# Kernel optimization log

Hardware: AMD Instinct MI355X
Metric: run time of the kernel (lower is better)

Reference implementation:

```python
import jax, jax.numpy as jnp
import numpy as np

LMAX = 5
DIMS = [2 * l + 1 for l in range(LMAX + 1)]
S = sum(d * d for d in DIMS)  # 286 = sum_l (2l+1)^2 (mul_l = dim_l = 2l+1)
F_IN, F_OUT = 128, 128
B = 512
N_GRID = 512


def setup_inputs() -> dict:
    key = jax.random.key(0)
    k1, k2, k3 = jax.random.split(key, 3)
    # x: signal over SO(3) irreps, shape (B, f_in, S)
    x = jax.random.normal(k1, (B, F_IN, S), dtype=jnp.float32)
    # w: learned spatial filter, shape (f_in, f_out, n_grid) (nn.Parameter, normal init)
    w = jax.random.normal(k2, (F_IN, F_OUT, N_GRID), dtype=jnp.float32)
    # D: flattened Wigner-D buffer, shape (n_grid, S). Stand-in random values;
    # the forward math is identical to the true Wigner-D buffer.
    D = jax.random.normal(k3, (N_GRID, S), dtype=jnp.float32)
    return {"x": x, "w": w, "D": D}


def _so3_linear(x, psi):
    """e3nn o3.Linear over so3_irreps(LMAX) with external weights psi.

    Per degree l: x_l (B, f_in, 2l+1 [mul], 2l+1 [dim]),
    psi_l (f_in, f_out, mul_in, mul_out); mix multiplicities and f channels,
    with fan-in normalization 1/sqrt(f_in * mul_in).
    """
    bsz = x.shape[0]
    outs = []
    off = 0
    for l in range(LMAX + 1):
        d = 2 * l + 1
        blk = d * d
        x_l = x[:, :, off:off + blk].reshape(bsz, F_IN, d, d)
        w_l = psi[:, :, off:off + blk].reshape(F_IN, F_OUT, d, d)
        scale = 1.0 / np.sqrt(F_IN * d).astype(np.float32)
        y_l = jnp.einsum('bxui,xyuv->byvi', x_l, w_l) * scale
        outs.append(y_l.reshape(bsz, F_OUT, blk))
        off += blk
    return jnp.concatenate(outs, axis=-1)


def reference(x, w, D):
    # project spatial filter into harmonic (Fourier) domain
    psi = jnp.einsum('ni,xyn->xyi', D, w) / np.float32(np.sqrt(N_GRID))
    return _so3_linear(x, psi)
```

## Files before the change

kernel.cpp:

```cpp
#include <hip/hip_runtime.h>
#include <hip/hip_bf16.h>


#define NT 256
#define NTILES 1144
#define NWORKERS 768
typedef __bf16 bf16x8 __attribute__((ext_vector_type(8)));
typedef float f32x4 __attribute__((ext_vector_type(4)));
typedef unsigned int u32;

__device__ __forceinline__ void gload_lds16(const void* g, void* l) {
  __builtin_amdgcn_global_load_lds(
      (const __attribute__((address_space(1))) u32*)g,
      (__attribute__((address_space(3))) u32*)l, 16, 0, 0);
}

__device__ __forceinline__ void decode_s(int s, int& off, int& d) {
  if (s >= 165)      { off = 165; d = 11; }
  else if (s >= 84)  { off = 84;  d = 9; }
  else if (s >= 35)  { off = 35;  d = 7; }
  else if (s >= 10)  { off = 10;  d = 5; }
  else if (s >= 1)   { off = 1;   d = 3; }
  else               { off = 0;   d = 1; }
}

__device__ __forceinline__ void stage_tile(
    const __hip_bfloat16* __restrict__ Ap, const __hip_bfloat16* __restrict__ Bp,
    int LDK, int ktv, int m0, int n0, int tid, int wave,
    __hip_bfloat16* sA, __hip_bfloat16* sB) {
#pragma unroll
  for (int c = 0; c < 4; ++c) {
    const int q = c * 256 + tid;
    const int row = q >> 3, slot = q & 7;
    const int scol = ((slot ^ (row & 7)) << 3);
    gload_lds16(&Ap[(m0 + row) * LDK + ktv + scol], &sA[(c * 256 + wave * 64) << 3]);
    gload_lds16(&Bp[(n0 + row) * LDK + ktv + scol], &sB[(c * 256 + wave * 64) << 3]);
  }
}

__device__ __forceinline__ void load_frags(
    const __hip_bfloat16* sA, const __hip_bfloat16* sB,
    int wr, int wc, int r15, int khi, bf16x8 (&af)[4][2], bf16x8 (&bf)[4][2]) {
#pragma unroll
  for (int m = 0; m < 4; ++m)
#pragma unroll
    for (int kk = 0; kk < 2; ++kk) {
      const int row = wr * 64 + m * 16 + r15;
      const int slot = (kk * 4 + khi) ^ (row & 7);
      af[m][kk] = *reinterpret_cast<const bf16x8*>(&sA[row * 64 + slot * 8]);
    }
#pragma unroll
  for (int n = 0; n < 4; ++n)
#pragma unroll
    for (int kk = 0; kk < 2; ++kk) {
      const int row = wc * 64 + n * 16 + r15;
      const int slot = (kk * 4 + khi) ^ (row & 7);
      bf[n][kk] = *reinterpret_cast<const bf16x8*>(&sB[row * 64 + slot * 8]);
    }
}

__device__ __forceinline__ void do_mfma(
    const bf16x8 (&af)[4][2], const bf16x8 (&bf)[4][2], f32x4 (&acc)[4][4]) {
#pragma unroll
  for (int kk = 0; kk < 2; ++kk)
#pragma unroll
    for (int m = 0; m < 4; ++m)
#pragma unroll
      for (int n = 0; n < 4; ++n)
        acc[m][n] = __builtin_amdgcn_mfma_f32_16x16x32_bf16(
            af[m][kk], bf[n][kk], acc[m][n], 0, 0, 0);
}

__global__ __launch_bounds__(NT)
void prep(const float* __restrict__ w, const float* __restrict__ Dm,
          __hip_bfloat16* __restrict__ wb, __hip_bfloat16* __restrict__ DT,
          int* __restrict__ cnt) {
  const int bx = blockIdx.x;
  if (bx == 0 && threadIdx.x == 0) *cnt = 0;
  if (bx < 4096) {
    const int t = bx * NT + threadIdx.x;
    const float4 a = reinterpret_cast<const float4*>(w)[t * 2];
    const float4 b = reinterpret_cast<const float4*>(w)[t * 2 + 1];
    __hip_bfloat16 v[8];
    v[0] = __float2bfloat16(a.x); v[1] = __float2bfloat16(a.y);
    v[2] = __float2bfloat16(a.z); v[3] = __float2bfloat16(a.w);
    v[4] = __float2bfloat16(b.x); v[5] = __float2bfloat16(b.y);
    v[6] = __float2bfloat16(b.z); v[7] = __float2bfloat16(b.w);
    *reinterpret_cast<bf16x8*>(&wb[t * 8]) = *reinterpret_cast<bf16x8*>(v);
  } else {
    const int e = (bx - 4096) * NT + threadIdx.x;
    const int s = e >> 9, g = e & 511;
    DT[e] = (s < 286) ? __float2bfloat16(Dm[g * 286 + s]) : __float2bfloat16(0.0f);
  }
}

__global__ __launch_bounds__(NT)
void psi_mfma(const __hip_bfloat16* __restrict__ wb,
              const __hip_bfloat16* __restrict__ DT,
              __hip_bfloat16* __restrict__ PT) {
  const int m0 = blockIdx.x * 128, n0 = blockIdx.y * 128;

  __shared__ __hip_bfloat16 sA[2][128 * 64];
  __shared__ __hip_bfloat16 sB[2][128 * 64];

  const int tid = threadIdx.x;
  const int lane = tid & 63, wave = tid >> 6;
  const int wr = wave & 1, wc = wave >> 1;
  const int r15 = lane & 15, khi = lane >> 4;

  f32x4 acc[4][4] = {};
  bf16x8 af[4][2], bf[4][2];

  stage_tile(wb, DT, 512, 0, m0, n0, tid, wave, sA[0], sB[0]);
  __syncthreads();
  int cur = 0;
  for (int t = 0; t < 8; ++t) {
    if (t + 1 < 8)
      stage_tile(wb, DT, 512, (t + 1) << 6, m0, n0, tid, wave, sA[cur ^ 1], sB[cur ^ 1]);
    load_frags(sA[cur], sB[cur], wr, wc, r15, khi, af, bf);
    do_mfma(af, bf, acc);
    if (t + 1 < 8) { __syncthreads(); cur ^= 1; }
  }

#pragma unroll
  for (int n = 0; n < 4; ++n) {
    const int s = n0 + wc * 64 + n * 16 + r15;
    if (s >= 286) continue;
    int off, d;
    decode_s(s, off, d);
    const int rel = s - off;
    const int u = rel / d, v = rel - u * d;
    const float scale = 1.0f / (256.0f * sqrtf((float)d));
    __hip_bfloat16* Pl = PT + off * 16384;
    const int Kd = 128 * d;
#pragma unroll
    for (int m = 0; m < 4; ++m)
#pragma unroll
      for (int j = 0; j < 4; ++j) {
        const int row = m0 + wr * 64 + m * 16 + khi * 4 + j;
        const int x = row >> 7, y = row & 127;
        Pl[(y * d + v) * Kd + (x * d + u)] = __float2bfloat16(acc[m][n][j] * scale);
      }
  }
}

template<int D, int OFF>
__device__ __forceinline__ void build_one(const float* __restrict__ X,
                                          __hip_bfloat16* __restrict__ A,
                                          int b, __hip_bfloat16* sm) {
  const float* src = X + (size_t)b * (128 * 286) + OFF;
  for (int e = threadIdx.x; e < 128 * D * D; e += NT) {
    const int x = e / (D * D), r = e - x * (D * D);
    sm[e] = __float2bfloat16(src[x * 286 + r]);
  }
  __syncthreads();
  __hip_bfloat16* dst = A + (size_t)65536 * OFF + (size_t)b * (D * 128 * D);
  for (int o = threadIdx.x; o < D * 128 * D; o += NT) {
    const int i = o / (128 * D);
    const int rem = o - i * (128 * D);
    const int x = rem / D, u = rem - x * D;
    dst[o] = sm[x * D * D + u * D + i];
  }
}

__global__ __launch_bounds__(NT)
void build_A_all(const float* __restrict__ X, __hip_bfloat16* __restrict__ A) {
  __shared__ __hip_bfloat16 sm[128 * 121];
  const int bx = blockIdx.x;
  if (bx < 512)       build_one<11, 165>(X, A, bx, sm);
  else if (bx < 1024) build_one<9, 84>(X, A, bx - 512, sm);
  else if (bx < 1536) build_one<7, 35>(X, A, bx - 1024, sm);
  else if (bx < 2048) build_one<5, 10>(X, A, bx - 1536, sm);
  else if (bx < 2560) build_one<3, 1>(X, A, bx - 2048, sm);
  else                build_one<1, 0>(X, A, bx - 2560, sm);
}

__global__ __launch_bounds__(NT)
void main_gemm(const __hip_bfloat16* __restrict__ Aall,
               const __hip_bfloat16* __restrict__ PTall,
               float* __restrict__ out, int* __restrict__ cnt) {
  __shared__ __hip_bfloat16 sA[128 * 64];
  __shared__ __hip_bfloat16 sB[128 * 64];
  __shared__ int s_tile;

  const int tid = threadIdx.x;
  const int lane = tid & 63, wave = tid >> 6;
  const int wr = wave & 1, wc = wave >> 1;
  const int r15 = lane & 15, khi = lane >> 4;

  for (;;) {
    if (tid == 0) s_tile = atomicAdd(cnt, 1);
    __syncthreads();
    int bx = s_tile;
    if (bx >= NTILES) return;

    int off, d;
    if (bx < 484)       { off = 165; d = 11; }
    else if (bx < 808)  { off = 84;  d = 9;  bx -= 484; }
    else if (bx < 1004) { off = 35;  d = 7;  bx -= 808; }
    else if (bx < 1104) { off = 10;  d = 5;  bx -= 1004; }
    else if (bx < 1140) { off = 1;   d = 3;  bx -= 1104; }
    else                { off = 0;   d = 1;  bx -= 1140; }
    const int bm = bx % (4 * d);
    const int bn = bx / (4 * d);
    const int Kn = 128 * d;
    const __hip_bfloat16* A  = Aall  + 65536 * off;
    const __hip_bfloat16* BT = PTall + 16384 * off;
    const int m0 = bm * 128, n0 = bn * 128;

    f32x4 acc[4][4] = {};
    bf16x8 af[4][2], bf[4][2];

    const int nk = Kn >> 6;
    for (int t = 0; t < nk; ++t) {
      stage_tile(A, BT, Kn, t << 6, m0, n0, tid, wave, sA, sB);
      __syncthreads();
      load_frags(sA, sB, wr, wc, r15, khi, af, bf);
      do_mfma(af, bf, acc);
      if (t + 1 < nk) __syncthreads();
    }

    int yo4[4], v4[4];
#pragma unroll
    for (int n = 0; n < 4; ++n) {
      const int col = n0 + wc * 64 + n * 16 + r15;
      yo4[n] = col / d;
      v4[n] = col - yo4[n] * d;
    }
#pragma unroll
    for (int m = 0; m < 4; ++m)
#pragma unroll
      for (int j = 0; j < 4; ++j) {
        const int row = m0 + wr * 64 + m * 16 + khi * 4 + j;
        const int bb = row / d, i = row - bb * d;
        float* orow = out + (size_t)bb * 36608 + off + i;
#pragma unroll
        for (int n = 0; n < 4; ++n)
          orow[yo4[n] * 286 + v4[n] * d] = acc[m][n][j];
      }
  }
}

extern "C" void kernel_launch(void* const* d_in, const int* in_sizes, int n_in,
                              void* d_out, int out_size, void* d_ws, size_t ws_size,
                              hipStream_t stream) {
  const float* x  = (const float*)d_in[0];
  const float* w  = (const float*)d_in[1];
  const float* Dm = (const float*)d_in[2];
  float* out = (float*)d_out;

  __hip_bfloat16* PT = (__hip_bfloat16*)d_ws;
  __hip_bfloat16* A  = PT + 16384 * 286;
  __hip_bfloat16* wb = A + 65536 * 286;
  __hip_bfloat16* DT = wb + 16384 * 512;
  int* cnt = (int*)(DT + 384 * 512);

  prep<<<dim3(4864), dim3(NT), 0, stream>>>(w, Dm, wb, DT, cnt);
  psi_mfma<<<dim3(128, 3), dim3(NT), 0, stream>>>(wb, DT, PT);
  build_A_all<<<dim3(3072), dim3(NT), 0, stream>>>(x, A);
  main_gemm<<<dim3(NWORKERS), dim3(NT), 0, stream>>>(A, PT, out, cnt);
}
```

Baseline: 167.3 us.

## Enlarge main GEMM tiles to 256x256 with 512-thread blocks and edge masking

The main GEMM moves from 128x128 tiles with 4 waves to 256x256 tiles with 8 waves, each wave computing a 128x64 sub-tile. Staging and fragment loads are inlined with an XOR swizzle. B rows past N are clamped and output columns past N are masked, because 128*d is not a multiple of 256. The aim is to raise data reuse and cut global/LDS traffic per FLOP. The cost is higher register use, padded wasted work, and fewer tiles (322) to spread across CUs.

Result: no change. 170.1 us (+1.7%).

```diff
diff --git a/kernel.cpp b/kernel.cpp
--- a/kernel.cpp
+++ b/kernel.cpp
@@ -3,8 +3,9 @@
 
 
 #define NT 256
-#define NTILES 1144
-#define NWORKERS 768
+#define NT2 512
+#define NTILES2 322
+#define NWORKERS 512
 typedef __bf16 bf16x8 __attribute__((ext_vector_type(8)));
 typedef float f32x4 __attribute__((ext_vector_type(4)));
 typedef unsigned int u32;
@@ -175,68 +176,105 @@
   else                build_one<1, 0>(X, A, bx - 2560, sm);
 }
 
-__global__ __launch_bounds__(NT)
+__global__ __launch_bounds__(NT2)
 void main_gemm(const __hip_bfloat16* __restrict__ Aall,
                const __hip_bfloat16* __restrict__ PTall,
                float* __restrict__ out, int* __restrict__ cnt) {
-  __shared__ __hip_bfloat16 sA[128 * 64];
-  __shared__ __hip_bfloat16 sB[128 * 64];
+  __shared__ __hip_bfloat16 sA[256 * 64];
+  __shared__ __hip_bfloat16 sB[256 * 64];
   __shared__ int s_tile;
 
   const int tid = threadIdx.x;
   const int lane = tid & 63, wave = tid >> 6;
-  const int wr = wave & 1, wc = wave >> 1;
+  const int wr = wave >> 2, wc = wave & 3;
   const int r15 = lane & 15, khi = lane >> 4;
 
   for (;;) {
     if (tid == 0) s_tile = atomicAdd(cnt, 1);
     __syncthreads();
     int bx = s_tile;
-    if (bx >= NTILES) return;
-
-    int off, d;
-    if (bx < 484)       { off = 165; d = 11; }
-    else if (bx < 808)  { off = 84;  d = 9;  bx -= 484; }
-    else if (bx < 1004) { off = 35;  d = 7;  bx -= 808; }
-    else if (bx < 1104) { off = 10;  d = 5;  bx -= 1004; }
-    else if (bx < 1140) { off = 1;   d = 3;  bx -= 1104; }
-    else                { off = 0;   d = 1;  bx -= 1140; }
-    const int bm = bx % (4 * d);
-    const int bn = bx / (4 * d);
-    const int Kn = 128 * d;
+    if (bx >= NTILES2) return;
+
+    int off, d, nbn;
+    if (bx < 132)      { off = 165; d = 11; nbn = 6; }
+    else if (bx < 222) { off = 84;  d = 9;  nbn = 5; bx -= 132; }
+    else if (bx < 278) { off = 35;  d = 7;  nbn = 4; bx -= 222; }
+    else if (bx < 308) { off = 10;  d = 5;  nbn = 3; bx -= 278; }
+    else if (bx < 320) { off = 1;   d = 3;  nbn = 2; bx -= 308; }
+    else               { off = 0;   d = 1;  nbn = 1; bx -= 320; }
+    const int bn = bx % nbn;
+    const int bm = bx / nbn;
+    const int Kn = 128 * d, Nn = 128 * d;
     const __hip_bfloat16* A  = Aall  + 65536 * off;
     const __hip_bfloat16* BT = PTall + 16384 * off;
-    const int m0 = bm * 128, n0 = bn * 128;
-
-    f32x4 acc[4][4] = {};
-    bf16x8 af[4][2], bf[4][2];
+    const int m0 = bm * 256, n0 = bn * 256;
+
+    f32x4 acc[8][4] = {};
 
     const int nk = Kn >> 6;
     for (int t = 0; t < nk; ++t) {
-      stage_tile(A, BT, Kn, t << 6, m0, n0, tid, wave, sA, sB);
+      const int kt = t << 6;
+#pragma unroll
+      for (int c = 0; c < 4; ++c) {
+        const int q = c * 512 + tid;
+        const int row = q >> 3, slot = q & 7;
+        const int scol = ((slot ^ (row & 7)) << 3);
+        gload_lds16(&A[(m0 + row) * Kn + kt + scol],
+                    &sA[(c * 512 + wave * 64) << 3]);
+        int brow = n0 + row;
+        if (brow >= Nn) brow = Nn - 1;
+        gload_lds16(&BT[brow * Kn + kt + scol],
+                    &sB[(c * 512 + wave * 64) << 3]);
+      }
       __syncthreads();
-      load_frags(sA, sB, wr, wc, r15, khi, af, bf);
-      do_mfma(af, bf, acc);
+
+      bf16x8 bfr[4][2];
+#pragma unroll
+      for (int n = 0; n < 4; ++n)
+#pragma unroll
+        for (int kk = 0; kk < 2; ++kk) {
+          const int row = wc * 64 + n * 16 + r15;
+          const int slot = (kk * 4 + khi) ^ (row & 7);
+          bfr[n][kk] = *reinterpret_cast<const bf16x8*>(&sB[row * 64 + slot * 8]);
+        }
+#pragma unroll
+      for (int m = 0; m < 8; ++m) {
+        bf16x8 afr[2];
+#pragma unroll
+        for (int kk = 0; kk < 2; ++kk) {
+          const int row = wr * 128 + m * 16 + r15;
+          const int slot = (kk * 4 + khi) ^ (row & 7);
+          afr[kk] = *reinterpret_cast<const bf16x8*>(&sA[row * 64 + slot * 8]);
+        }
+#pragma unroll
+        for (int kk = 0; kk < 2; ++kk)
+#pragma unroll
+          for (int n = 0; n < 4; ++n)
+            acc[m][n] = __builtin_amdgcn_mfma_f32_16x16x32_bf16(
+                afr[kk], bfr[n][kk], acc[m][n], 0, 0, 0);
+      }
       if (t + 1 < nk) __syncthreads();
     }
 
-    int yo4[4], v4[4];
+    int yo4[4], v4[4], cok[4];
 #pragma unroll
     for (int n = 0; n < 4; ++n) {
       const int col = n0 + wc * 64 + n * 16 + r15;
-      yo4[n] = col / d;
-      v4[n] = col - yo4[n] * d;
+      cok[n] = (col < Nn);
+      const int cc = cok[n] ? col : 0;
+      yo4[n] = cc / d;
+      v4[n] = cc - yo4[n] * d;
     }
 #pragma unroll
-    for (int m = 0; m < 4; ++m)
+    for (int m = 0; m < 8; ++m)
 #pragma unroll
       for (int j = 0; j < 4; ++j) {
-        const int row = m0 + wr * 64 + m * 16 + khi * 4 + j;
+        const int row = m0 + wr * 128 + m * 16 + khi * 4 + j;
         const int bb = row / d, i = row - bb * d;
         float* orow = out + (size_t)bb * 36608 + off + i;
 #pragma unroll
         for (int n = 0; n < 4; ++n)
-          orow[yo4[n] * 286 + v4[n] * d] = acc[m][n][j];
+          if (cok[n]) orow[yo4[n] * 286 + v4[n] * d] = acc[m][n][j];
       }
   }
 }
@@ -258,5 +296,5 @@
   prep<<<dim3(4864), dim3(NT), 0, stream>>>(w, Dm, wb, DT, cnt);
   psi_mfma<<<dim3(128, 3), dim3(NT), 0, stream>>>(wb, DT, PT);
   build_A_all<<<dim3(3072), dim3(NT), 0, stream>>>(x, A);
-  main_gemm<<<dim3(NWORKERS), dim3(NT), 0, stream>>>(A, PT, out, cnt);
-}
+  main_gemm<<<dim3(NWORKERS), dim3(NT2), 0, stream>>>(A, PT, out, cnt);
+}
```

## Stage GEMM epilogue through LDS for coalesced writes, fuse A-build into prep

Applied to the files above, without the earlier changes.

The main GEMM epilogue now writes accumulators to a padded LDS buffer and scatters them to global memory in output-index order, so stores to the strided output layout coalesce better than direct per-lane scattered stores. The tile body is templated on degree so K and loop counts become compile-time constants. The separate build_A kernel is merged into the prep kernel, removing one launch. LDS use rises to about 33KB and extra synchronisation plus a bounds-checked loop are added in the epilogue.

After: 179.4 us. 7.2% more time.

```diff
diff --git a/kernel.cpp b/kernel.cpp
--- a/kernel.cpp
+++ b/kernel.cpp
@@ -24,57 +24,31 @@
   else               { off = 0;   d = 1; }
 }
 
-__device__ __forceinline__ void stage_tile(
-    const __hip_bfloat16* __restrict__ Ap, const __hip_bfloat16* __restrict__ Bp,
-    int LDK, int ktv, int m0, int n0, int tid, int wave,
-    __hip_bfloat16* sA, __hip_bfloat16* sB) {
-#pragma unroll
-  for (int c = 0; c < 4; ++c) {
-    const int q = c * 256 + tid;
-    const int row = q >> 3, slot = q & 7;
-    const int scol = ((slot ^ (row & 7)) << 3);
-    gload_lds16(&Ap[(m0 + row) * LDK + ktv + scol], &sA[(c * 256 + wave * 64) << 3]);
-    gload_lds16(&Bp[(n0 + row) * LDK + ktv + scol], &sB[(c * 256 + wave * 64) << 3]);
-  }
-}
-
-__device__ __forceinline__ void load_frags(
-    const __hip_bfloat16* sA, const __hip_bfloat16* sB,
-    int wr, int wc, int r15, int khi, bf16x8 (&af)[4][2], bf16x8 (&bf)[4][2]) {
-#pragma unroll
-  for (int m = 0; m < 4; ++m)
-#pragma unroll
-    for (int kk = 0; kk < 2; ++kk) {
-      const int row = wr * 64 + m * 16 + r15;
-      const int slot = (kk * 4 + khi) ^ (row & 7);
-      af[m][kk] = *reinterpret_cast<const bf16x8*>(&sA[row * 64 + slot * 8]);
-    }
-#pragma unroll
-  for (int n = 0; n < 4; ++n)
-#pragma unroll
-    for (int kk = 0; kk < 2; ++kk) {
-      const int row = wc * 64 + n * 16 + r15;
-      const int slot = (kk * 4 + khi) ^ (row & 7);
-      bf[n][kk] = *reinterpret_cast<const bf16x8*>(&sB[row * 64 + slot * 8]);
-    }
-}
-
-__device__ __forceinline__ void do_mfma(
-    const bf16x8 (&af)[4][2], const bf16x8 (&bf)[4][2], f32x4 (&acc)[4][4]) {
-#pragma unroll
-  for (int kk = 0; kk < 2; ++kk)
-#pragma unroll
-    for (int m = 0; m < 4; ++m)
-#pragma unroll
-      for (int n = 0; n < 4; ++n)
-        acc[m][n] = __builtin_amdgcn_mfma_f32_16x16x32_bf16(
-            af[m][kk], bf[n][kk], acc[m][n], 0, 0, 0);
+template<int D, int OFF>
+__device__ __forceinline__ void build_one(const float* __restrict__ X,
+                                          __hip_bfloat16* __restrict__ A,
+                                          int b, __hip_bfloat16* sm) {
+  const float* src = X + (size_t)b * (128 * 286) + OFF;
+  for (int e = threadIdx.x; e < 128 * D * D; e += NT) {
+    const int x = e / (D * D), r = e - x * (D * D);
+    sm[e] = __float2bfloat16(src[x * 286 + r]);
+  }
+  __syncthreads();
+  __hip_bfloat16* dst = A + (size_t)65536 * OFF + (size_t)b * (D * 128 * D);
+  for (int o = threadIdx.x; o < D * 128 * D; o += NT) {
+    const int i = o / (128 * D);
+    const int rem = o - i * (128 * D);
+    const int x = rem / D, u = rem - x * D;
+    dst[o] = sm[x * D * D + u * D + i];
+  }
 }
 
 __global__ __launch_bounds__(NT)
-void prep(const float* __restrict__ w, const float* __restrict__ Dm,
-          __hip_bfloat16* __restrict__ wb, __hip_bfloat16* __restrict__ DT,
-          int* __restrict__ cnt) {
+void prep_all(const float* __restrict__ w, const float* __restrict__ Dm,
+              const float* __restrict__ X,
+              __hip_bfloat16* __restrict__ wb, __hip_bfloat16* __restrict__ DT,
+              __hip_bfloat16* __restrict__ A, int* __restrict__ cnt) {
+  __shared__ __hip_bfloat16 sm[128 * 121];
   const int bx = blockIdx.x;
   if (bx == 0 && threadIdx.x == 0) *cnt = 0;
   if (bx < 4096) {
@@ -87,11 +61,66 @@
     v[4] = __float2bfloat16(b.x); v[5] = __float2bfloat16(b.y);
     v[6] = __float2bfloat16(b.z); v[7] = __float2bfloat16(b.w);
     *reinterpret_cast<bf16x8*>(&wb[t * 8]) = *reinterpret_cast<bf16x8*>(v);
-  } else {
+  } else if (bx < 4864) {
     const int e = (bx - 4096) * NT + threadIdx.x;
     const int s = e >> 9, g = e & 511;
     DT[e] = (s < 286) ? __float2bfloat16(Dm[g * 286 + s]) : __float2bfloat16(0.0f);
-  }
+  } else {
+    const int b2 = bx - 4864;
+    if (b2 < 512)       build_one<11, 165>(X, A, b2, sm);
+    else if (b2 < 1024) build_one<9, 84>(X, A, b2 - 512, sm);
+    else if (b2 < 1536) build_one<7, 35>(X, A, b2 - 1024, sm);
+    else if (b2 < 2048) build_one<5, 10>(X, A, b2 - 1536, sm);
+    else if (b2 < 2560) build_one<3, 1>(X, A, b2 - 2048, sm);
+    else                build_one<1, 0>(X, A, b2 - 2560, sm);
+  }
+}
+
+__device__ __forceinline__ void stage_tile(
+    const __hip_bfloat16* __restrict__ Ap, const __hip_bfloat16* __restrict__ Bp,
+    int LDK, int ktv, int m0, int n0, int tid, int wave,
+    __hip_bfloat16* sA, __hip_bfloat16* sB) {
+#pragma unroll
+  for (int c = 0; c < 4; ++c) {
+    const int q = c * 256 + tid;
+    const int row = q >> 3, slot = q & 7;
+    const int scol = ((slot ^ (row & 7)) << 3);
+    gload_lds16(&Ap[(m0 + row) * LDK + ktv + scol], &sA[(c * 256 + wave * 64) << 3]);
+    gload_lds16(&Bp[(n0 + row) * LDK + ktv + scol], &sB[(c * 256 + wave * 64) << 3]);
+  }
+}
+
+__device__ __forceinline__ void load_frags(
+    const __hip_bfloat16* sA, const __hip_bfloat16* sB,
+    int wr, int wc, int r15, int khi, bf16x8 (&af)[4][2], bf16x8 (&bf)[4][2]) {
+#pragma unroll
+  for (int m = 0; m < 4; ++m)
+#pragma unroll
+    for (int kk = 0; kk < 2; ++kk) {
+      const int row = wr * 64 + m * 16 + r15;
+      const int slot = (kk * 4 + khi) ^ (row & 7);
+      af[m][kk] = *reinterpret_cast<const bf16x8*>(&sA[row * 64 + slot * 8]);
+    }
+#pragma unroll
+  for (int n = 0; n < 4; ++n)
+#pragma unroll
+    for (int kk = 0; kk < 2; ++kk) {
+      const int row = wc * 64 + n * 16 + r15;
+      const int slot = (kk * 4 + khi) ^ (row & 7);
+      bf[n][kk] = *reinterpret_cast<const bf16x8*>(&sB[row * 64 + slot * 8]);
+    }
+}
+
+__device__ __forceinline__ void do_mfma(
+    const bf16x8 (&af)[4][2], const bf16x8 (&bf)[4][2], f32x4 (&acc)[4][4]) {
+#pragma unroll
+  for (int kk = 0; kk < 2; ++kk)
+#pragma unroll
+    for (int m = 0; m < 4; ++m)
+#pragma unroll
+      for (int n = 0; n < 4; ++n)
+        acc[m][n] = __builtin_amdgcn_mfma_f32_16x16x32_bf16(
+            af[m][kk], bf[n][kk], acc[m][n], 0, 0, 0);
 }
 
 __global__ __launch_bounds__(NT)
@@ -145,99 +174,105 @@
 }
 
 template<int D, int OFF>
-__device__ __forceinline__ void build_one(const float* __restrict__ X,
-                                          __hip_bfloat16* __restrict__ A,
-                                          int b, __hip_bfloat16* sm) {
-  const float* src = X + (size_t)b * (128 * 286) + OFF;
-  for (int e = threadIdx.x; e < 128 * D * D; e += NT) {
-    const int x = e / (D * D), r = e - x * (D * D);
-    sm[e] = __float2bfloat16(src[x * 286 + r]);
-  }
-  __syncthreads();
-  __hip_bfloat16* dst = A + (size_t)65536 * OFF + (size_t)b * (D * 128 * D);
-  for (int o = threadIdx.x; o < D * 128 * D; o += NT) {
-    const int i = o / (128 * D);
-    const int rem = o - i * (128 * D);
-    const int x = rem / D, u = rem - x * D;
-    dst[o] = sm[x * D * D + u * D + i];
-  }
-}
-
-__global__ __launch_bounds__(NT)
-void build_A_all(const float* __restrict__ X, __hip_bfloat16* __restrict__ A) {
-  __shared__ __hip_bfloat16 sm[128 * 121];
-  const int bx = blockIdx.x;
-  if (bx < 512)       build_one<11, 165>(X, A, bx, sm);
-  else if (bx < 1024) build_one<9, 84>(X, A, bx - 512, sm);
-  else if (bx < 1536) build_one<7, 35>(X, A, bx - 1024, sm);
-  else if (bx < 2048) build_one<5, 10>(X, A, bx - 1536, sm);
-  else if (bx < 2560) build_one<3, 1>(X, A, bx - 2048, sm);
-  else                build_one<1, 0>(X, A, bx - 2560, sm);
+__device__ __forceinline__ void tile_body(
+    const __hip_bfloat16* __restrict__ Aall,
+    const __hip_bfloat16* __restrict__ PTall,
+    float* __restrict__ out, int bx,
+    __hip_bfloat16* sA, __hip_bfloat16* sB, float* sE) {
+  const int tid = threadIdx.x;
+  const int lane = tid & 63, wave = tid >> 6;
+  const int wr = wave & 1, wc = wave >> 1;
+  const int r15 = lane & 15, khi = lane >> 4;
+
+  constexpr int Kn = 128 * D;
+  constexpr int nk = 2 * D;
+  const int bm = bx % (4 * D);
+  const int bn = bx / (4 * D);
+  const __hip_bfloat16* A  = Aall  + 65536 * OFF;
+  const __hip_bfloat16* BT = PTall + 16384 * OFF;
+  const int m0 = bm * 128, n0 = bn * 128;
+
+  f32x4 acc[4][4] = {};
+  bf16x8 af[4][2], bf[4][2];
+
+  for (int t = 0; t < nk; ++t) {
+    const int kt = t << 6;
+#pragma unroll
+    for (int c = 0; c < 4; ++c) {
+      const int q = c * 256 + tid;
+      const int row = q >> 3, slot = q & 7;
+      const int scol = ((slot ^ (row & 7)) << 3);
+      gload_lds16(&A[(m0 + row) * Kn + kt + scol], &sA[(c * 256 + wave * 64) << 3]);
+      gload_lds16(&BT[(n0 + row) * Kn + kt + scol], &sB[(c * 256 + wave * 64) << 3]);
+    }
+    __syncthreads();
+    load_frags(sA, sB, wr, wc, r15, khi, af, bf);
+    do_mfma(af, bf, acc);
+    __syncthreads();
+  }
+
+#pragma unroll
+  for (int ch = 0; ch < 2; ++ch) {
+    if (wr == ch) {
+#pragma unroll
+      for (int m = 0; m < 4; ++m)
+#pragma unroll
+        for (int j = 0; j < 4; ++j) {
+          const int lr = m * 16 + khi * 4 + j;
+#pragma unroll
+          for (int n = 0; n < 4; ++n) {
+            const int c = wc * 64 + n * 16 + r15;
+            sE[lr * 129 + c] = acc[m][n][j];
+          }
+        }
+    }
+    __syncthreads();
+    const int base_row = m0 + ch * 64;
+    const int b_lo = base_row / D;
+    const int yo_lo = n0 / D;
+    constexpr int NBMAX = 64 / D + 2;
+    constexpr int NYOC = 128 / D + 2;
+    constexpr int TOT = NBMAX * NYOC * D * D;
+    for (int e = tid; e < TOT; e += NT) {
+      const int s = e % (D * D);
+      const int t2 = e / (D * D);
+      const int yos = t2 % NYOC;
+      const int bs = t2 / NYOC;
+      const int b = b_lo + bs;
+      const int yo = yo_lo + yos;
+      const int i = s % D, v = s / D;
+      const int row = b * D + i;
+      const int col = yo * D + v;
+      if (row < base_row || row >= base_row + 64) continue;
+      if (col < n0 || col >= n0 + 128) continue;
+      out[(size_t)b * 36608 + yo * 286 + OFF + v * D + i] =
+          sE[(row - base_row) * 129 + (col - n0)];
+    }
+    __syncthreads();
+  }
 }
 
 __global__ __launch_bounds__(NT)
 void main_gemm(const __hip_bfloat16* __restrict__ Aall,
                const __hip_bfloat16* __restrict__ PTall,
                float* __restrict__ out, int* __restrict__ cnt) {
-  __shared__ __hip_bfloat16 sA[128 * 64];
-  __shared__ __hip_bfloat16 sB[128 * 64];
+  __shared__ __align__(16) unsigned char smem[33024];
   __shared__ int s_tile;
-
-  const int tid = threadIdx.x;
-  const int lane = tid & 63, wave = tid >> 6;
-  const int wr = wave & 1, wc = wave >> 1;
-  const int r15 = lane & 15, khi = lane >> 4;
+  __hip_bfloat16* sA = (__hip_bfloat16*)smem;
+  __hip_bfloat16* sB = (__hip_bfloat16*)(smem + 16384);
+  float* sE = (float*)smem;
 
   for (;;) {
-    if (tid == 0) s_tile = atomicAdd(cnt, 1);
-    __syncthreads();
-    int bx = s_tile;
+    if (threadIdx.x == 0) s_tile = atomicAdd(cnt, 1);
+    __syncthreads();
+    const int bx = s_tile;
     if (bx >= NTILES) return;
-
-    int off, d;
-    if (bx < 484)       { off = 165; d = 11; }
-    else if (bx < 808)  { off = 84;  d = 9;  bx -= 484; }
-    else if (bx < 1004) { off = 35;  d = 7;  bx -= 808; }
-    else if (bx < 1104) { off = 10;  d = 5;  bx -= 1004; }
-    else if (bx < 1140) { off = 1;   d = 3;  bx -= 1104; }
-    else                { off = 0;   d = 1;  bx -= 1140; }
-    const int bm = bx % (4 * d);
-    const int bn = bx / (4 * d);
-    const int Kn = 128 * d;
-    const __hip_bfloat16* A  = Aall  + 65536 * off;
-    const __hip_bfloat16* BT = PTall + 16384 * off;
-    const int m0 = bm * 128, n0 = bn * 128;
-
-    f32x4 acc[4][4] = {};
-    bf16x8 af[4][2], bf[4][2];
-
-    const int nk = Kn >> 6;
-    for (int t = 0; t < nk; ++t) {
-      stage_tile(A, BT, Kn, t << 6, m0, n0, tid, wave, sA, sB);
-      __syncthreads();
-      load_frags(sA, sB, wr, wc, r15, khi, af, bf);
-      do_mfma(af, bf, acc);
-      if (t + 1 < nk) __syncthreads();
-    }
-
-    int yo4[4], v4[4];
-#pragma unroll
-    for (int n = 0; n < 4; ++n) {
-      const int col = n0 + wc * 64 + n * 16 + r15;
-      yo4[n] = col / d;
-      v4[n] = col - yo4[n] * d;
-    }
-#pragma unroll
-    for (int m = 0; m < 4; ++m)
-#pragma unroll
-      for (int j = 0; j < 4; ++j) {
-        const int row = m0 + wr * 64 + m * 16 + khi * 4 + j;
-        const int bb = row / d, i = row - bb * d;
-        float* orow = out + (size_t)bb * 36608 + off + i;
-#pragma unroll
-        for (int n = 0; n < 4; ++n)
-          orow[yo4[n] * 286 + v4[n] * d] = acc[m][n][j];
-      }
+    if (bx < 484)       tile_body<11, 165>(Aall, PTall, out, bx, sA, sB, sE);
+    else if (bx < 808)  tile_body<9, 84>(Aall, PTall, out, bx - 484, sA, sB, sE);
+    else if (bx < 1004) tile_body<7, 35>(Aall, PTall, out, bx - 808, sA, sB, sE);
+    else if (bx < 1104) tile_body<5, 10>(Aall, PTall, out, bx - 1004, sA, sB, sE);
+    else if (bx < 1140) tile_body<3, 1>(Aall, PTall, out, bx - 1104, sA, sB, sE);
+    else                tile_body<1, 0>(Aall, PTall, out, bx - 1140, sA, sB, sE);
   }
 }
 
@@ -255,8 +290,7 @@
   __hip_bfloat16* DT = wb + 16384 * 512;
   int* cnt = (int*)(DT + 384 * 512);
 
-  prep<<<dim3(4864), dim3(NT), 0, stream>>>(w, Dm, wb, DT, cnt);
+  prep_all<<<dim3(7936), dim3(NT), 0, stream>>>(w, Dm, x, wb, DT, A, cnt);
   psi_mfma<<<dim3(128, 3), dim3(NT), 0, stream>>>(wb, DT, PT);
-  build_A_all<<<dim3(3072), dim3(NT), 0, stream>>>(x, A);
   main_gemm<<<dim3(NWORKERS), dim3(NT), 0, stream>>>(A, PT, out, cnt);
 }
```
